# Kernel optimization log

Hardware: AMD Instinct MI355X
Metric: run time of the kernel (lower is better)

The kernel has to match this reference:

```python
import jax, jax.numpy as jnp
import numpy as np

EPS = 1e-6

def setup_inputs() -> dict:
    key = jax.random.key(0)
    k1, k2, k3 = jax.random.split(key, 3)
    B, C, H, W = 8, 384, 32, 32
    dim = C
    x = jax.random.normal(k1, (B, C, H, W), dtype=jnp.float32)
    # torch Linear weights: [out_features, in_features]
    w_qkv = jax.random.normal(k2, (3 * dim, dim), dtype=jnp.float32) * (dim ** -0.5)
    w_proj = jax.random.normal(k3, (dim, dim), dtype=jnp.float32) * (dim ** -0.5)
    ln_w = jnp.ones((dim,), dtype=jnp.float32)
    ln_b = jnp.zeros((dim,), dtype=jnp.float32)
    return {"x": x, "w_qkv": w_qkv, "w_proj": w_proj, "ln_w": ln_w, "ln_b": ln_b}

def reference(x, w_qkv, w_proj, ln_w, ln_b):
    num_heads = 8
    B, C, H, W = x.shape
    N = H * W
    head_dim = C // num_heads
    scale = head_dim ** -0.5

    tokens = jnp.transpose(x, (0, 2, 3, 1)).reshape(B, N, C)  # [B,N,C]
    residual = tokens
    # LayerNorm over last dim
    mu = jnp.mean(tokens, axis=-1, keepdims=True)
    var = jnp.mean(jnp.square(tokens - mu), axis=-1, keepdims=True)
    t = (tokens - mu) * jax.lax.rsqrt(var + EPS) * ln_w + ln_b

    qkv = t @ w_qkv.T                                  # [B,N,3C]
    qkv = qkv.reshape(B, N, 3, num_heads, head_dim)
    qkv = jnp.transpose(qkv, (2, 0, 3, 1, 4))          # [3,B,h,N,d]
    q, k, v = qkv[0], qkv[1], qkv[2]

    attn = jnp.einsum('bhnd,bhmd->bhnm', q, k) * scale  # [B,h,N,N]
    attn = jax.nn.softmax(attn, axis=-1)
    out = jnp.einsum('bhnm,bhmd->bhnd', attn, v)        # [B,h,N,d]
    out = jnp.transpose(out, (0, 2, 1, 3)).reshape(B, N, C)
    out = out @ w_proj.T
    out = residual + out
    return jnp.transpose(out.reshape(B, H, W, C), (0, 3, 1, 2))
```

## Files before the change

kernel.cpp:

```cpp
#include <hip/hip_runtime.h>
#include <math.h>

typedef __attribute__((ext_vector_type(4))) float f32x4;
typedef __attribute__((ext_vector_type(8))) short s16x8;

constexpr int B_ = 8, C_ = 384, N_ = 1024, NH_ = 8, D_ = 48;
constexpr float SCALE_ = 0.14433756729740643f;

__device__ __forceinline__ unsigned short f2bf(float f) {
    unsigned u = __builtin_bit_cast(unsigned, f);
    u += 0x7fff + ((u >> 16) & 1);
    return (unsigned short)(u >> 16);
}
__device__ __forceinline__ unsigned short f2bf_trunc(float f) {
    return (unsigned short)(__builtin_bit_cast(unsigned, f) >> 16);
}

__global__ __launch_bounds__(256) void ln_cvt_kernel(const float* __restrict__ x,
                                                     const float* __restrict__ lnw,
                                                     const float* __restrict__ lnb,
                                                     const float* __restrict__ wq,
                                                     const float* __restrict__ wp,
                                                     unsigned short* __restrict__ t,
                                                     unsigned short* __restrict__ wqb,
                                                     unsigned short* __restrict__ wpb) {
    int tid = threadIdx.x;
    int gid = blockIdx.x * 256 + tid;
    for (int i = gid; i < 1152 * 384; i += 512 * 256) wqb[i] = f2bf(wq[i]);
    for (int i = gid; i < 384 * 384;  i += 512 * 256) wpb[i] = f2bf(wp[i]);

    __shared__ float xs[384][17];
    __shared__ float wgt[384], bia[384];
    int b  = blockIdx.x >> 6;
    int n0 = (blockIdx.x & 63) << 4;
    for (int i = tid; i < 384; i += 256) { wgt[i] = lnw[i]; bia[i] = lnb[i]; }

    const float* xb = x + (size_t)b * 384 * 1024;
    #pragma unroll
    for (int k = 0; k < 24; k++) {
        int f = tid + k * 256;
        int c = f >> 4, l = f & 15;
        xs[c][l] = xb[(size_t)c * 1024 + n0 + l];
    }
    __syncthreads();

    int l = tid >> 4, part = tid & 15;
    float s = 0.f, sq = 0.f;
    #pragma unroll
    for (int j = 0; j < 24; j++) {
        float v = xs[part + j * 16][l];
        s += v; sq += v * v;
    }
    #pragma unroll
    for (int off = 1; off <= 8; off <<= 1) {
        s  += __shfl_xor(s,  off);
        sq += __shfl_xor(sq, off);
    }
    float mu   = s * (1.0f / 384.0f);
    float rstd = rsqrtf(sq * (1.0f / 384.0f) - mu * mu + 1e-6f);

    unsigned short* tp = t + (size_t)(b * 1024 + n0 + l) * 384 + part * 24;
    #pragma unroll
    for (int m = 0; m < 24; m++) {
        int c = part * 24 + m;
        tp[m] = f2bf((xs[c][l] - mu) * rstd * wgt[c] + bia[c]);
    }
}

__global__ __launch_bounds__(256) void qkv_mfma(const unsigned short* __restrict__ t,
                                                const unsigned short* __restrict__ w,
                                                unsigned short* __restrict__ qb,
                                                unsigned short* __restrict__ kb,
                                                unsigned short* __restrict__ vt) {
    __shared__ __align__(16) unsigned short As[128][40];
    __shared__ __align__(16) unsigned short Bs[128][40];

    int tid = threadIdx.x;
    int m0 = blockIdx.x * 128;
    int j0 = blockIdx.y * 128;
    int lane = tid & 63, wid = tid >> 6;
    int wr = wid >> 1, wc = wid & 1;
    int q16 = lane & 15, quad = lane >> 4;

    f32x4 acc[4][4] = {};

    const int srow = tid >> 2, spart = (tid & 3) * 8;
    for (int k0 = 0; k0 < 384; k0 += 32) {
        *(int4*)&As[srow][spart]      = *(const int4*)&t[(size_t)(m0 + srow) * 384 + k0 + spart];
        *(int4*)&As[srow + 64][spart] = *(const int4*)&t[(size_t)(m0 + srow + 64) * 384 + k0 + spart];
        *(int4*)&Bs[srow][spart]      = *(const int4*)&w[(size_t)(j0 + srow) * 384 + k0 + spart];
        *(int4*)&Bs[srow + 64][spart] = *(const int4*)&w[(size_t)(j0 + srow + 64) * 384 + k0 + spart];
        __syncthreads();
        s16x8 af[4], bfr[4];
        #pragma unroll
        for (int mi = 0; mi < 4; mi++) af[mi]  = *(const s16x8*)&As[wr * 64 + mi * 16 + q16][quad * 8];
        #pragma unroll
        for (int ni = 0; ni < 4; ni++) bfr[ni] = *(const s16x8*)&Bs[wc * 64 + ni * 16 + q16][quad * 8];
        #pragma unroll
        for (int mi = 0; mi < 4; mi++)
            #pragma unroll
            for (int ni = 0; ni < 4; ni++)
                acc[mi][ni] = __builtin_amdgcn_mfma_f32_16x16x32_bf16(af[mi], bfr[ni], acc[mi][ni], 0, 0, 0);
        __syncthreads();
    }

    #pragma unroll
    for (int mi = 0; mi < 4; mi++) {
        int m_base = m0 + wr * 64 + mi * 16 + quad * 4;
        int bb = m_base >> 10;
        int nn = m_base & 1023;
        #pragma unroll
        for (int ni = 0; ni < 4; ni++) {
            int col = j0 + wc * 64 + ni * 16 + q16;
            int which = col / 384;
            int c2 = col - which * 384;
            int head = c2 / 48;
            int dd = c2 - head * 48;
            f32x4 a = acc[mi][ni];
            if (which == 0) {
                size_t base = (((size_t)bb * 8 + head) * 1024 + nn) * 48 + dd;
                qb[base      ] = f2bf(a.x * SCALE_);
                qb[base +  48] = f2bf(a.y * SCALE_);
                qb[base +  96] = f2bf(a.z * SCALE_);
                qb[base + 144] = f2bf(a.w * SCALE_);
            } else if (which == 1) {
                size_t base = (((size_t)bb * 8 + head) * 1024 + nn) * 48 + dd;
                kb[base      ] = f2bf(a.x);
                kb[base +  48] = f2bf(a.y);
                kb[base +  96] = f2bf(a.z);
                kb[base + 144] = f2bf(a.w);
            } else {
                size_t base = (((size_t)bb * 8 + head) * 48 + dd) * 1024 + nn;
                ushort4 v4 = { f2bf(a.x), f2bf(a.y), f2bf(a.z), f2bf(a.w) };
                *(ushort4*)&vt[base] = v4;
            }
        }
    }
}

__global__ __launch_bounds__(256) void attn_mfma(const unsigned short* __restrict__ qb,
                                                 const unsigned short* __restrict__ kb,
                                                 const unsigned short* __restrict__ vt,
                                                 unsigned short* __restrict__ ao) {
    __shared__ __align__(16) unsigned short Qs[64][72];
    __shared__ __align__(16) unsigned short Ks[128][72];
    __shared__ __align__(16) unsigned short Vt[48][136];

    unsigned short* Ps = &Ks[0][0];

    int tid = threadIdx.x, lane = tid & 63, wid = tid >> 6;
    int q16 = lane & 15, quad = lane >> 4;
    int qt = blockIdx.x, h = blockIdx.y, b = blockIdx.z;
    size_t hb = (size_t)b * NH_ + h;
    const unsigned short* qp = qb + hb * N_ * 48;
    const unsigned short* kp = kb + hb * N_ * 48;
    const unsigned short* vp = vt + hb * 48 * N_;

    int4 z4 = {0, 0, 0, 0};
    if (tid < 64) { *(int4*)&Qs[tid][48] = z4; *(int4*)&Qs[tid][56] = z4; }

    if (tid < 128) {
        int r = tid >> 1, off = (tid & 1) * 24;
        const unsigned short* gp = qp + (size_t)(qt * 64 + r) * 48 + off;
        *(int4*)&Qs[r][off]      = *(const int4*)gp;
        *(int4*)&Qs[r][off + 8]  = *(const int4*)(gp + 8);
        *(int4*)&Qs[r][off + 16] = *(const int4*)(gp + 16);
    }
    __syncthreads();

    s16x8 qf0 = *(const s16x8*)&Qs[wid * 16 + q16][quad * 8];
    s16x8 qf1 = *(const s16x8*)&Qs[wid * 16 + q16][32 + quad * 8];

    f32x4 o[3] = {};
    float mrow[4], lrow[4];
    #pragma unroll
    for (int r = 0; r < 4; r++) { mrow[r] = -1e30f; lrow[r] = 0.f; }

    for (int kt = 0; kt < 8; kt++) {
        {
            int r = tid >> 1, off = (tid & 1) * 24;
            const unsigned short* gp = kp + (size_t)(kt * 128 + r) * 48 + off;
            *(int4*)&Ks[r][off]      = *(const int4*)gp;
            *(int4*)&Ks[r][off + 8]  = *(const int4*)(gp + 8);
            *(int4*)&Ks[r][off + 16] = *(const int4*)(gp + 16);
            if ((tid & 1) == 0) { *(int4*)&Ks[r][48] = z4; *(int4*)&Ks[r][56] = z4; }
        }
        for (int i = tid; i < 768; i += 256) {
            int r = i >> 4, c = (i & 15) * 8;
            *(int4*)&Vt[r][c] = *(const int4*)&vp[(size_t)r * 1024 + kt * 128 + c];
        }
        __syncthreads();

        f32x4 s[8];
        #pragma unroll
        for (int nt = 0; nt < 8; nt++) {
            s16x8 k0 = *(const s16x8*)&Ks[nt * 16 + q16][quad * 8];
            s16x8 k1 = *(const s16x8*)&Ks[nt * 16 + q16][32 + quad * 8];
            f32x4 z = {};
            z = __builtin_amdgcn_mfma_f32_16x16x32_bf16(qf0, k0, z, 0, 0, 0);
            z = __builtin_amdgcn_mfma_f32_16x16x32_bf16(qf1, k1, z, 0, 0, 0);
            s[nt] = z;
        }
        __syncthreads();

        float al[4];
        #pragma unroll
        for (int r = 0; r < 4; r++) {
            float m1 = s[0][r];
            #pragma unroll
            for (int nt = 1; nt < 8; nt++) m1 = fmaxf(m1, s[nt][r]);
            #pragma unroll
            for (int off = 1; off <= 8; off <<= 1) m1 = fmaxf(m1, __shfl_xor(m1, off));
            float mn = fmaxf(mrow[r], m1);
            al[r] = __expf(mrow[r] - mn);
            mrow[r] = mn;
            float sum = 0.f;
            #pragma unroll
            for (int nt = 0; nt < 8; nt++) {
                float p = __expf(s[nt][r] - mn);
                s[nt][r] = p;
                sum += p;
            }
            #pragma unroll
            for (int off = 1; off <= 8; off <<= 1) sum += __shfl_xor(sum, off);
            lrow[r] = lrow[r] * al[r] + sum;
        }

        #pragma unroll
        for (int nt = 0; nt < 8; nt++)
            #pragma unroll
            for (int r = 0; r < 4; r++)
                Ps[(wid * 16 + quad * 4 + r) * 136 + nt * 16 + q16] = f2bf_trunc(s[nt][r]);

        #pragma unroll
        for (int dt = 0; dt < 3; dt++)
            #pragma unroll
            for (int r = 0; r < 4; r++)
                o[dt][r] *= al[r];

        #pragma unroll
        for (int c = 0; c < 4; c++) {
            s16x8 pf = *(const s16x8*)&Ps[(wid * 16 + q16) * 136 + c * 32 + quad * 8];
            #pragma unroll
            for (int dt = 0; dt < 3; dt++) {
                s16x8 vf = *(const s16x8*)&Vt[dt * 16 + q16][c * 32 + quad * 8];
                o[dt] = __builtin_amdgcn_mfma_f32_16x16x32_bf16(pf, vf, o[dt], 0, 0, 0);
            }
        }
        __syncthreads();
    }

    float inv[4];
    #pragma unroll
    for (int r = 0; r < 4; r++) inv[r] = __builtin_amdgcn_rcpf(lrow[r]);
    #pragma unroll
    for (int dt = 0; dt < 3; dt++)
        #pragma unroll
        for (int r = 0; r < 4; r++)
            Qs[wid * 16 + quad * 4 + r][dt * 16 + q16] = f2bf(o[dt][r] * inv[r]);
    __syncthreads();

    if (tid < 128) {
        int r = tid >> 1, off = (tid & 1) * 24;
        unsigned short* dst = ao + ((size_t)b * 1024 + qt * 64 + r) * 384 + h * 48 + off;
        *(int4*)dst        = *(const int4*)&Qs[r][off];
        *(int4*)(dst + 8)  = *(const int4*)&Qs[r][off + 8];
        *(int4*)(dst + 16) = *(const int4*)&Qs[r][off + 16];
    }
}

__global__ __launch_bounds__(256) void proj_mfma(const unsigned short* __restrict__ ao,
                                                 const unsigned short* __restrict__ w,
                                                 const float* __restrict__ x,
                                                 float* __restrict__ out) {
    __shared__ __align__(16) unsigned short As[64][40];
    __shared__ __align__(16) unsigned short Bs[128][40];

    int tid = threadIdx.x;
    int m0 = blockIdx.x * 64;
    int j0 = blockIdx.y * 128;
    int lane = tid & 63, wid = tid >> 6;
    int wr = wid >> 1, wc = wid & 1;
    int q16 = lane & 15, quad = lane >> 4;

    f32x4 acc[2][4] = {};

    const int srowA = tid >> 2, spartA = (tid & 3) * 8;
    const int srowB = tid >> 1, spartB = (tid & 1) * 16;
    for (int k0 = 0; k0 < 384; k0 += 32) {
        *(int4*)&As[srowA][spartA]     = *(const int4*)&ao[(size_t)(m0 + srowA) * 384 + k0 + spartA];
        *(int4*)&Bs[srowB][spartB]     = *(const int4*)&w[(size_t)(j0 + srowB) * 384 + k0 + spartB];
        *(int4*)&Bs[srowB][spartB + 8] = *(const int4*)&w[(size_t)(j0 + srowB) * 384 + k0 + spartB + 8];
        __syncthreads();
        s16x8 af[2], bfr[4];
        #pragma unroll
        for (int mi = 0; mi < 2; mi++) af[mi]  = *(const s16x8*)&As[wr * 32 + mi * 16 + q16][quad * 8];
        #pragma unroll
        for (int ni = 0; ni < 4; ni++) bfr[ni] = *(const s16x8*)&Bs[wc * 64 + ni * 16 + q16][quad * 8];
        #pragma unroll
        for (int mi = 0; mi < 2; mi++)
            #pragma unroll
            for (int ni = 0; ni < 4; ni++)
                acc[mi][ni] = __builtin_amdgcn_mfma_f32_16x16x32_bf16(af[mi], bfr[ni], acc[mi][ni], 0, 0, 0);
        __syncthreads();
    }

    #pragma unroll
    for (int mi = 0; mi < 2; mi++) {
        int m_base = m0 + wr * 32 + mi * 16 + quad * 4;
        int bb = m_base >> 10;
        int nn = m_base & 1023;
        #pragma unroll
        for (int ni = 0; ni < 4; ni++) {
            int col = j0 + wc * 64 + ni * 16 + q16;
            size_t idx = ((size_t)bb * 384 + col) * 1024 + nn;
            float4 xr = *(const float4*)&x[idx];
            f32x4 a = acc[mi][ni];
            float4 ov = { xr.x + a.x, xr.y + a.y, xr.z + a.z, xr.w + a.w };
            *(float4*)&out[idx] = ov;
        }
    }
}

extern "C" void kernel_launch(void* const* d_in, const int* in_sizes, int n_in,
                              void* d_out, int out_size, void* d_ws, size_t ws_size,
                              hipStream_t stream) {
    const float* x     = (const float*)d_in[0];
    const float* wqkv  = (const float*)d_in[1];
    const float* wproj = (const float*)d_in[2];
    const float* lnw   = (const float*)d_in[3];
    const float* lnb   = (const float*)d_in[4];
    float* out = (float*)d_out;

    unsigned short* ws16 = (unsigned short*)d_ws;
    size_t off = 0;
    unsigned short* t_bf  = ws16 + off; off += (size_t)8192 * 384;
    unsigned short* wq_bf = ws16 + off; off += (size_t)1152 * 384;
    unsigned short* wp_bf = ws16 + off; off += (size_t)384 * 384;
    unsigned short* qb    = ws16 + off; off += (size_t)64 * 1024 * 48;
    unsigned short* kb    = ws16 + off; off += (size_t)64 * 1024 * 48;
    unsigned short* vt    = ws16 + off; off += (size_t)64 * 48 * 1024;
    unsigned short* ao_bf = ws16 + off; off += (size_t)8192 * 384;

    ln_cvt_kernel<<<512, 256, 0, stream>>>(x, lnw, lnb, wqkv, wproj, t_bf, wq_bf, wp_bf);
    qkv_mfma<<<dim3(64, 9), 256, 0, stream>>>(t_bf, wq_bf, qb, kb, vt);
    attn_mfma<<<dim3(16, NH_, B_), 256, 0, stream>>>(qb, kb, vt, ao_bf);
    proj_mfma<<<dim3(128, 3), 256, 0, stream>>>(ao_bf, wp_bf, x, out);
}
```

Baseline: 160.8 us.

## Coalesce Q/K stores via LDS staging, use token-major Q/K layout, double K-step

The QKV GEMM epilogue for Q and K now stages the bf16 tile in shared memory and writes 16-byte coalesced rows into a token-major [B,N,384] layout, replacing scattered 2-byte stores into a per-head layout. Attention reads Q and K with a 384-element row stride and reuses the K smem buffer for Q staging, which removes the separate Qs array and lowers LDS use. Both GEMMs move from a K-step of 32 to 64, halving the number of barrier iterations at the cost of larger shared tiles. The strided Q/K reads in attention are less contiguous than the old per-head layout.

After: 160.0 us. No clear change (-0.5%).

```diff
diff --git a/kernel.cpp b/kernel.cpp
--- a/kernel.cpp
+++ b/kernel.cpp
@@ -69,67 +69,89 @@
 
 __global__ __launch_bounds__(256) void qkv_mfma(const unsigned short* __restrict__ t,
                                                 const unsigned short* __restrict__ w,
-                                                unsigned short* __restrict__ qb,
-                                                unsigned short* __restrict__ kb,
+                                                unsigned short* __restrict__ qn,
+                                                unsigned short* __restrict__ kn,
                                                 unsigned short* __restrict__ vt) {
-    __shared__ __align__(16) unsigned short As[128][40];
-    __shared__ __align__(16) unsigned short Bs[128][40];
+    __shared__ __align__(16) unsigned short As[128][72];
+    __shared__ __align__(16) unsigned short Bs[128][72];
 
     int tid = threadIdx.x;
     int m0 = blockIdx.x * 128;
-    int j0 = blockIdx.y * 128;
+    int jb = blockIdx.y;
+    int j0 = jb * 128;
     int lane = tid & 63, wid = tid >> 6;
     int wr = wid >> 1, wc = wid & 1;
     int q16 = lane & 15, quad = lane >> 4;
 
     f32x4 acc[4][4] = {};
 
-    const int srow = tid >> 2, spart = (tid & 3) * 8;
-    for (int k0 = 0; k0 < 384; k0 += 32) {
-        *(int4*)&As[srow][spart]      = *(const int4*)&t[(size_t)(m0 + srow) * 384 + k0 + spart];
-        *(int4*)&As[srow + 64][spart] = *(const int4*)&t[(size_t)(m0 + srow + 64) * 384 + k0 + spart];
-        *(int4*)&Bs[srow][spart]      = *(const int4*)&w[(size_t)(j0 + srow) * 384 + k0 + spart];
-        *(int4*)&Bs[srow + 64][spart] = *(const int4*)&w[(size_t)(j0 + srow + 64) * 384 + k0 + spart];
-        __syncthreads();
-        s16x8 af[4], bfr[4];
-        #pragma unroll
-        for (int mi = 0; mi < 4; mi++) af[mi]  = *(const s16x8*)&As[wr * 64 + mi * 16 + q16][quad * 8];
-        #pragma unroll
-        for (int ni = 0; ni < 4; ni++) bfr[ni] = *(const s16x8*)&Bs[wc * 64 + ni * 16 + q16][quad * 8];
-        #pragma unroll
-        for (int mi = 0; mi < 4; mi++)
-            #pragma unroll
-            for (int ni = 0; ni < 4; ni++)
-                acc[mi][ni] = __builtin_amdgcn_mfma_f32_16x16x32_bf16(af[mi], bfr[ni], acc[mi][ni], 0, 0, 0);
-        __syncthreads();
-    }
-
-    #pragma unroll
-    for (int mi = 0; mi < 4; mi++) {
-        int m_base = m0 + wr * 64 + mi * 16 + quad * 4;
-        int bb = m_base >> 10;
-        int nn = m_base & 1023;
-        #pragma unroll
-        for (int ni = 0; ni < 4; ni++) {
-            int col = j0 + wc * 64 + ni * 16 + q16;
-            int which = col / 384;
-            int c2 = col - which * 384;
-            int head = c2 / 48;
-            int dd = c2 - head * 48;
-            f32x4 a = acc[mi][ni];
-            if (which == 0) {
-                size_t base = (((size_t)bb * 8 + head) * 1024 + nn) * 48 + dd;
-                qb[base      ] = f2bf(a.x * SCALE_);
-                qb[base +  48] = f2bf(a.y * SCALE_);
-                qb[base +  96] = f2bf(a.z * SCALE_);
-                qb[base + 144] = f2bf(a.w * SCALE_);
-            } else if (which == 1) {
-                size_t base = (((size_t)bb * 8 + head) * 1024 + nn) * 48 + dd;
-                kb[base      ] = f2bf(a.x);
-                kb[base +  48] = f2bf(a.y);
-                kb[base +  96] = f2bf(a.z);
-                kb[base + 144] = f2bf(a.w);
-            } else {
+    const int srow = tid >> 1, sc0 = (tid & 1) * 32;
+    for (int k0 = 0; k0 < 384; k0 += 64) {
+        const unsigned short* ga = &t[(size_t)(m0 + srow) * 384 + k0 + sc0];
+        const unsigned short* gb = &w[(size_t)(j0 + srow) * 384 + k0 + sc0];
+        *(int4*)&As[srow][sc0]      = *(const int4*)(ga);
+        *(int4*)&As[srow][sc0 + 8]  = *(const int4*)(ga + 8);
+        *(int4*)&As[srow][sc0 + 16] = *(const int4*)(ga + 16);
+        *(int4*)&As[srow][sc0 + 24] = *(const int4*)(ga + 24);
+        *(int4*)&Bs[srow][sc0]      = *(const int4*)(gb);
+        *(int4*)&Bs[srow][sc0 + 8]  = *(const int4*)(gb + 8);
+        *(int4*)&Bs[srow][sc0 + 16] = *(const int4*)(gb + 16);
+        *(int4*)&Bs[srow][sc0 + 24] = *(const int4*)(gb + 24);
+        __syncthreads();
+        #pragma unroll
+        for (int s = 0; s < 2; s++) {
+            s16x8 af[4], bfr[4];
+            #pragma unroll
+            for (int mi = 0; mi < 4; mi++) af[mi]  = *(const s16x8*)&As[wr * 64 + mi * 16 + q16][s * 32 + quad * 8];
+            #pragma unroll
+            for (int ni = 0; ni < 4; ni++) bfr[ni] = *(const s16x8*)&Bs[wc * 64 + ni * 16 + q16][s * 32 + quad * 8];
+            #pragma unroll
+            for (int mi = 0; mi < 4; mi++)
+                #pragma unroll
+                for (int ni = 0; ni < 4; ni++)
+                    acc[mi][ni] = __builtin_amdgcn_mfma_f32_16x16x32_bf16(af[mi], bfr[ni], acc[mi][ni], 0, 0, 0);
+        }
+        __syncthreads();
+    }
+
+    if (jb < 6) {
+        unsigned short (*Cs)[136] = (unsigned short (*)[136])&As[0][0];
+        const float sc = (jb < 3) ? SCALE_ : 1.0f;
+        unsigned short* dst = (jb < 3) ? qn : kn;
+        int coff = (jb < 3 ? jb : jb - 3) * 128;
+        #pragma unroll
+        for (int p = 0; p < 2; p++) {
+            if (wr == p) {
+                #pragma unroll
+                for (int mi = 0; mi < 4; mi++)
+                    #pragma unroll
+                    for (int ni = 0; ni < 4; ni++)
+                        #pragma unroll
+                        for (int r = 0; r < 4; r++)
+                            Cs[mi * 16 + quad * 4 + r][wc * 64 + ni * 16 + q16] = f2bf(acc[mi][ni][r] * sc);
+            }
+            __syncthreads();
+            #pragma unroll
+            for (int i = tid; i < 1024; i += 256) {
+                int rr = i >> 4, cc = (i & 15) * 8;
+                int m = m0 + p * 64 + rr;
+                int bsel = m >> 10, nn = m & 1023;
+                *(int4*)&dst[(size_t)(bsel * 1024 + nn) * 384 + coff + cc] = *(const int4*)&Cs[rr][cc];
+            }
+            __syncthreads();
+        }
+    } else {
+        #pragma unroll
+        for (int mi = 0; mi < 4; mi++) {
+            int m_base = m0 + wr * 64 + mi * 16 + quad * 4;
+            int bb = m_base >> 10;
+            int nn = m_base & 1023;
+            #pragma unroll
+            for (int ni = 0; ni < 4; ni++) {
+                int c2 = (jb - 6) * 128 + wc * 64 + ni * 16 + q16;
+                int head = c2 / 48;
+                int dd = c2 - head * 48;
+                f32x4 a = acc[mi][ni];
                 size_t base = (((size_t)bb * 8 + head) * 48 + dd) * 1024 + nn;
                 ushort4 v4 = { f2bf(a.x), f2bf(a.y), f2bf(a.z), f2bf(a.w) };
                 *(ushort4*)&vt[base] = v4;
@@ -138,11 +160,10 @@
     }
 }
 
-__global__ __launch_bounds__(256) void attn_mfma(const unsigned short* __restrict__ qb,
-                                                 const unsigned short* __restrict__ kb,
+__global__ __launch_bounds__(256) void attn_mfma(const unsigned short* __restrict__ qn,
+                                                 const unsigned short* __restrict__ kn,
                                                  const unsigned short* __restrict__ vt,
                                                  unsigned short* __restrict__ ao) {
-    __shared__ __align__(16) unsigned short Qs[64][72];
     __shared__ __align__(16) unsigned short Ks[128][72];
     __shared__ __align__(16) unsigned short Vt[48][136];
 
@@ -151,25 +172,25 @@
     int tid = threadIdx.x, lane = tid & 63, wid = tid >> 6;
     int q16 = lane & 15, quad = lane >> 4;
     int qt = blockIdx.x, h = blockIdx.y, b = blockIdx.z;
-    size_t hb = (size_t)b * NH_ + h;
-    const unsigned short* qp = qb + hb * N_ * 48;
-    const unsigned short* kp = kb + hb * N_ * 48;
-    const unsigned short* vp = vt + hb * 48 * N_;
+    const unsigned short* qp = qn + (size_t)b * 1024 * 384 + h * 48;
+    const unsigned short* kp = kn + (size_t)b * 1024 * 384 + h * 48;
+    const unsigned short* vp = vt + ((size_t)b * NH_ + h) * 48 * N_;
 
     int4 z4 = {0, 0, 0, 0};
-    if (tid < 64) { *(int4*)&Qs[tid][48] = z4; *(int4*)&Qs[tid][56] = z4; }
 
     if (tid < 128) {
         int r = tid >> 1, off = (tid & 1) * 24;
-        const unsigned short* gp = qp + (size_t)(qt * 64 + r) * 48 + off;
-        *(int4*)&Qs[r][off]      = *(const int4*)gp;
-        *(int4*)&Qs[r][off + 8]  = *(const int4*)(gp + 8);
-        *(int4*)&Qs[r][off + 16] = *(const int4*)(gp + 16);
+        const unsigned short* gp = qp + (size_t)(qt * 64 + r) * 384 + off;
+        *(int4*)&Ks[r][off]      = *(const int4*)gp;
+        *(int4*)&Ks[r][off + 8]  = *(const int4*)(gp + 8);
+        *(int4*)&Ks[r][off + 16] = *(const int4*)(gp + 16);
+        if ((tid & 1) == 0) { *(int4*)&Ks[r][48] = z4; *(int4*)&Ks[r][56] = z4; }
     }
     __syncthreads();
 
-    s16x8 qf0 = *(const s16x8*)&Qs[wid * 16 + q16][quad * 8];
-    s16x8 qf1 = *(const s16x8*)&Qs[wid * 16 + q16][32 + quad * 8];
+    s16x8 qf0 = *(const s16x8*)&Ks[wid * 16 + q16][quad * 8];
+    s16x8 qf1 = *(const s16x8*)&Ks[wid * 16 + q16][32 + quad * 8];
+    __syncthreads();
 
     f32x4 o[3] = {};
     float mrow[4], lrow[4];
@@ -179,7 +200,7 @@
     for (int kt = 0; kt < 8; kt++) {
         {
             int r = tid >> 1, off = (tid & 1) * 24;
-            const unsigned short* gp = kp + (size_t)(kt * 128 + r) * 48 + off;
+            const unsigned short* gp = kp + (size_t)(kt * 128 + r) * 384 + off;
             *(int4*)&Ks[r][off]      = *(const int4*)gp;
             *(int4*)&Ks[r][off + 8]  = *(const int4*)(gp + 8);
             *(int4*)&Ks[r][off + 16] = *(const int4*)(gp + 16);
@@ -257,15 +278,15 @@
     for (int dt = 0; dt < 3; dt++)
         #pragma unroll
         for (int r = 0; r < 4; r++)
-            Qs[wid * 16 + quad * 4 + r][dt * 16 + q16] = f2bf(o[dt][r] * inv[r]);
+            Ks[wid * 16 + quad * 4 + r][dt * 16 + q16] = f2bf(o[dt][r] * inv[r]);
     __syncthreads();
 
     if (tid < 128) {
         int r = tid >> 1, off = (tid & 1) * 24;
         unsigned short* dst = ao + ((size_t)b * 1024 + qt * 64 + r) * 384 + h * 48 + off;
-        *(int4*)dst        = *(const int4*)&Qs[r][off];
-        *(int4*)(dst + 8)  = *(const int4*)&Qs[r][off + 8];
-        *(int4*)(dst + 16) = *(const int4*)&Qs[r][off + 16];
+        *(int4*)dst        = *(const int4*)&Ks[r][off];
+        *(int4*)(dst + 8)  = *(const int4*)&Ks[r][off + 8];
+        *(int4*)(dst + 16) = *(const int4*)&Ks[r][off + 16];
     }
 }
 
@@ -273,8 +294,8 @@
                                                  const unsigned short* __restrict__ w,
                                                  const float* __restrict__ x,
                                                  float* __restrict__ out) {
-    __shared__ __align__(16) unsigned short As[64][40];
-    __shared__ __align__(16) unsigned short Bs[128][40];
+    __shared__ __align__(16) unsigned short As[64][72];
+    __shared__ __align__(16) unsigned short Bs[128][72];
 
     int tid = threadIdx.x;
     int m0 = blockIdx.x * 64;
@@ -285,23 +306,31 @@
 
     f32x4 acc[2][4] = {};
 
-    const int srowA = tid >> 2, spartA = (tid & 3) * 8;
-    const int srowB = tid >> 1, spartB = (tid & 1) * 16;
-    for (int k0 = 0; k0 < 384; k0 += 32) {
-        *(int4*)&As[srowA][spartA]     = *(const int4*)&ao[(size_t)(m0 + srowA) * 384 + k0 + spartA];
-        *(int4*)&Bs[srowB][spartB]     = *(const int4*)&w[(size_t)(j0 + srowB) * 384 + k0 + spartB];
-        *(int4*)&Bs[srowB][spartB + 8] = *(const int4*)&w[(size_t)(j0 + srowB) * 384 + k0 + spartB + 8];
-        __syncthreads();
-        s16x8 af[2], bfr[4];
-        #pragma unroll
-        for (int mi = 0; mi < 2; mi++) af[mi]  = *(const s16x8*)&As[wr * 32 + mi * 16 + q16][quad * 8];
-        #pragma unroll
-        for (int ni = 0; ni < 4; ni++) bfr[ni] = *(const s16x8*)&Bs[wc * 64 + ni * 16 + q16][quad * 8];
-        #pragma unroll
-        for (int mi = 0; mi < 2; mi++)
-            #pragma unroll
-            for (int ni = 0; ni < 4; ni++)
-                acc[mi][ni] = __builtin_amdgcn_mfma_f32_16x16x32_bf16(af[mi], bfr[ni], acc[mi][ni], 0, 0, 0);
+    const int srowA = tid >> 2, scA = (tid & 3) * 16;
+    const int srowB = tid >> 1, scB = (tid & 1) * 32;
+    for (int k0 = 0; k0 < 384; k0 += 64) {
+        const unsigned short* ga = &ao[(size_t)(m0 + srowA) * 384 + k0 + scA];
+        const unsigned short* gb = &w[(size_t)(j0 + srowB) * 384 + k0 + scB];
+        *(int4*)&As[srowA][scA]     = *(const int4*)(ga);
+        *(int4*)&As[srowA][scA + 8] = *(const int4*)(ga + 8);
+        *(int4*)&Bs[srowB][scB]      = *(const int4*)(gb);
+        *(int4*)&Bs[srowB][scB + 8]  = *(const int4*)(gb + 8);
+        *(int4*)&Bs[srowB][scB + 16] = *(const int4*)(gb + 16);
+        *(int4*)&Bs[srowB][scB + 24] = *(const int4*)(gb + 24);
+        __syncthreads();
+        #pragma unroll
+        for (int s = 0; s < 2; s++) {
+            s16x8 af[2], bfr[4];
+            #pragma unroll
+            for (int mi = 0; mi < 2; mi++) af[mi]  = *(const s16x8*)&As[wr * 32 + mi * 16 + q16][s * 32 + quad * 8];
+            #pragma unroll
+            for (int ni = 0; ni < 4; ni++) bfr[ni] = *(const s16x8*)&Bs[wc * 64 + ni * 16 + q16][s * 32 + quad * 8];
+            #pragma unroll
+            for (int mi = 0; mi < 2; mi++)
+                #pragma unroll
+                for (int ni = 0; ni < 4; ni++)
+                    acc[mi][ni] = __builtin_amdgcn_mfma_f32_16x16x32_bf16(af[mi], bfr[ni], acc[mi][ni], 0, 0, 0);
+        }
         __syncthreads();
     }
 
@@ -337,13 +366,13 @@
     unsigned short* t_bf  = ws16 + off; off += (size_t)8192 * 384;
     unsigned short* wq_bf = ws16 + off; off += (size_t)1152 * 384;
     unsigned short* wp_bf = ws16 + off; off += (size_t)384 * 384;
-    unsigned short* qb    = ws16 + off; off += (size_t)64 * 1024 * 48;
-    unsigned short* kb    = ws16 + off; off += (size_t)64 * 1024 * 48;
+    unsigned short* qn    = ws16 + off; off += (size_t)8192 * 384;
+    unsigned short* kn    = ws16 + off; off += (size_t)8192 * 384;
     unsigned short* vt    = ws16 + off; off += (size_t)64 * 48 * 1024;
     unsigned short* ao_bf = ws16 + off; off += (size_t)8192 * 384;
 
     ln_cvt_kernel<<<512, 256, 0, stream>>>(x, lnw, lnb, wqkv, wproj, t_bf, wq_bf, wp_bf);
-    qkv_mfma<<<dim3(64, 9), 256, 0, stream>>>(t_bf, wq_bf, qb, kb, vt);
-    attn_mfma<<<dim3(16, NH_, B_), 256, 0, stream>>>(qb, kb, vt, ao_bf);
+    qkv_mfma<<<dim3(64, 9), 256, 0, stream>>>(t_bf, wq_bf, qn, kn, vt);
+    attn_mfma<<<dim3(16, NH_, B_), 256, 0, stream>>>(qn, kn, vt, ao_bf);
     proj_mfma<<<dim3(128, 3), 256, 0, stream>>>(ao_bf, wp_bf, x, out);
 }
```
